# Kernel optimization log

Measured on AMD Instinct MI355X. Metric: run time of the kernel, lower is better.

The kernel has to match this reference:

```python
import jax, jax.numpy as jnp
import numpy as np

N_NODES = 50000


def gcn_conv(x, W, b, src, dst, n_nodes):
    """PyG GCNConv: x' = D^-1/2 (A+I) D^-1/2 (x W) + b (symmetric norm, self-loops)."""
    h = x @ W  # [N, out]
    loop = jnp.arange(n_nodes, dtype=src.dtype)
    src_f = jnp.concatenate([src, loop])
    dst_f = jnp.concatenate([dst, loop])
    ones = jnp.ones(src_f.shape[0], dtype=h.dtype)
    deg = jax.ops.segment_sum(ones, dst_f, num_segments=n_nodes)
    dinv = jnp.where(deg > 0, jax.lax.rsqrt(deg), 0.0)
    norm = dinv[src_f] * dinv[dst_f]  # [E+N]
    msg = h[src_f] * norm[:, None]    # irregular gather over edges
    out = jax.ops.segment_sum(msg, dst_f, num_segments=n_nodes)
    return out + b


def setup_inputs() -> dict:
    key = jax.random.key(0)
    ks = jax.random.split(key, 9)
    d_in, d_h = 128, 128
    x = jax.random.normal(ks[0], (N_NODES, d_in), dtype=jnp.float32)
    edge_index = jax.random.randint(ks[1], (2, 800000), 0, N_NODES, dtype=jnp.int64)
    glorot = lambda k, fi, fo: jax.random.normal(k, (fi, fo), dtype=jnp.float32) * jnp.sqrt(2.0 / (fi + fo))
    return {
        "x": x,
        "edge_index": edge_index,
        "W1": glorot(ks[2], d_in, d_h), "b1": jnp.zeros((d_h,), jnp.float32),
        "W2": glorot(ks[3], d_h, d_h), "b2": jnp.zeros((d_h,), jnp.float32),
        "W3": glorot(ks[4], d_h, d_h), "b3": jnp.zeros((d_h,), jnp.float32),
    }


def reference(x, edge_index, W1, b1, W2, b2, W3, b3):
    src, dst = edge_index[0], edge_index[1]
    n = x.shape[0]
    h = jax.nn.relu(gcn_conv(x, W1, b1, src, dst, n))
    h = jax.nn.relu(gcn_conv(h, W2, b2, src, dst, n))
    h = gcn_conv(h, W3, b3, src, dst, n)
    return h
```

## Files before the change

kernel.cpp:

```cpp
#include <hip/hip_runtime.h>

#define N_NODES 50000
#define N_EDGES 800000
#define DIM 128
#define WT_BLOCKS 192
#define GEMM_BLOCKS ((N_NODES + 63) / 64)
#define NBUCKET ((N_NODES + 255) / 256)
#define P1_BLOCKS 200
#define P1_CHUNK 4000
#define P2_BLOCKS 200
#define P2_CHUNK 4000

typedef unsigned int u32;
typedef short bf16x8 __attribute__((ext_vector_type(8)));
typedef float f32x4 __attribute__((ext_vector_type(4)));

static inline size_t alignUp(size_t x) { return (x + 255) & ~size_t(255); }

__device__ inline unsigned short f2bf(float f) {
    union { float f; u32 u; } v; v.f = f;
    u32 r = v.u + 0x7fffu + ((v.u >> 16) & 1u);
    return (unsigned short)(r >> 16);
}
__device__ inline float bf_lo(u32 u) { return __uint_as_float(u << 16); }
__device__ inline float bf_hi(u32 u) { return __uint_as_float(u & 0xffff0000u); }

__device__ inline void accum8(float acc[8], uint4 r, float w) {
    acc[0] += w * bf_lo(r.x); acc[1] += w * bf_hi(r.x);
    acc[2] += w * bf_lo(r.y); acc[3] += w * bf_hi(r.y);
    acc[4] += w * bf_lo(r.z); acc[5] += w * bf_hi(r.z);
    acc[6] += w * bf_lo(r.w); acc[7] += w * bf_hi(r.w);
}

__global__ __launch_bounds__(256) void prep_kernel(const float* __restrict__ W1,
                                                   const float* __restrict__ W2,
                                                   const float* __restrict__ W3,
                                                   unsigned short* __restrict__ Wt,
                                                   const int* __restrict__ dst,
                                                   u32* __restrict__ bcnt) {
    __shared__ u32 hist[NBUCKET];
    int bid = blockIdx.x;
    if (bid < WT_BLOCKS) {
        int m = bid >> 6;
        int e = (bid & 63) * 256 + threadIdx.x;
        int n = e >> 7, k = e & 127;
        const float* W = (m == 0) ? W1 : (m == 1) ? W2 : W3;
        Wt[m * DIM * DIM + n * DIM + k] = f2bf(W[(size_t)k * DIM + n]);
        return;
    }
    int b = bid - WT_BLOCKS;
    for (int k = threadIdx.x; k < NBUCKET; k += 256) hist[k] = 0;
    __syncthreads();
    int e0 = b * P1_CHUNK;
    int e1 = min(e0 + P1_CHUNK, N_EDGES);
    for (int i = e0 + threadIdx.x; i < e1; i += 256)
        atomicAdd(&hist[((u32)dst[i]) >> 8], 1u);
    __syncthreads();
    for (int k = threadIdx.x; k < NBUCKET; k += 256)
        if (hist[k]) atomicAdd(&bcnt[k], hist[k]);
}

__global__ __launch_bounds__(256) void part_kernel(const int* __restrict__ src,
                                                   const int* __restrict__ dst,
                                                   const u32* __restrict__ bcnt,
                                                   u32* __restrict__ bcur,
                                                   u32* __restrict__ epart) {
    __shared__ u32 ed[P2_CHUNK];
    __shared__ u32 hist[NBUCKET];
    __shared__ u32 cb[NBUCKET];
    __shared__ u32 rk[NBUCKET];
    __shared__ u32 bb[256];
    __shared__ u32 wsum[4];
    int tid = threadIdx.x, lane = tid & 63, wv = tid >> 6;
    u32 c = (tid < NBUCKET) ? bcnt[tid] : 0;
    u32 v = c;
#pragma unroll
    for (int off = 1; off < 64; off <<= 1) {
        u32 u = __shfl_up(v, off, 64);
        if (lane >= off) v += u;
    }
    if (lane == 63) wsum[wv] = v;
    for (int k = tid; k < NBUCKET; k += 256) { hist[k] = 0; rk[k] = 0; }
    __syncthreads();
    u32 wo = 0;
    for (int w = 0; w < wv; w++) wo += wsum[w];
    bb[tid] = wo + v - c;
    __syncthreads();
    int e0 = blockIdx.x * P2_CHUNK;
    int e1 = min(e0 + P2_CHUNK, N_EDGES);
    for (int i = e0 + tid; i < e1; i += 256) {
        u32 s = (u32)src[i], d = (u32)dst[i];
        u32 val = s | (d << 16);
        ed[i - e0] = val;
        atomicAdd(&hist[d >> 8], 1u);
    }
    __syncthreads();
    for (int k = tid; k < NBUCKET; k += 256) {
        u32 ck = hist[k];
        cb[k] = ck ? (bb[k] + atomicAdd(&bcur[k], ck)) : 0u;
    }
    __syncthreads();
    int n = e1 - e0;
    for (int k = tid; k < n; k += 256) {
        u32 val = ed[k];
        u32 bk = val >> 24;
        u32 r = atomicAdd(&rk[bk], 1u);
        epart[cb[bk] + r] = val;
    }
}

#define LDSTRIDE 40
__global__ __launch_bounds__(256) void gemm_mfma_kernel(const float* __restrict__ x,
                                                        const unsigned short* __restrict__ xb,
                                                        const unsigned short* __restrict__ Wt,
                                                        unsigned short* __restrict__ hb,
                                                        int n_rows,
                                                        const u32* __restrict__ bcnt,
                                                        const u32* __restrict__ epart,
                                                        int* __restrict__ cnt,
                                                        int* __restrict__ base,
                                                        float* __restrict__ dinv,
                                                        unsigned short* __restrict__ csr16) {
    __shared__ unsigned short As[64 * LDSTRIDE];
    __shared__ unsigned short Bs[128 * LDSTRIDE];
    if (blockIdx.x >= GEMM_BLOCKS) {
        int B = blockIdx.x - GEMM_BLOCKS;
        u32* hcnt = (u32*)&As[0];
        u32* pref = hcnt + 256;
        u32* bbl  = pref + 256;
        u32* wsum = bbl + 256;
        int tid = threadIdx.x, lane = tid & 63, wv = tid >> 6;
        int nb0 = B << 8;
        u32 cb_ = (tid < NBUCKET) ? bcnt[tid] : 0;
        u32 vb = cb_;
#pragma unroll
        for (int off = 1; off < 64; off <<= 1) {
            u32 u = __shfl_up(vb, off, 64);
            if (lane >= off) vb += u;
        }
        if (lane == 63) wsum[wv] = vb;
        hcnt[tid] = 0;
        __syncthreads();
        u32 wob = 0;
        for (int w = 0; w < wv; w++) wob += wsum[w];
        bbl[tid] = wob + vb - cb_;
        __syncthreads();
        u32 ebeg = bbl[B];
        u32 esz  = bcnt[B];
        for (u32 k = tid; k < esz; k += 256)
            atomicAdd(&hcnt[(epart[ebeg + k] >> 16) & 255u], 1u);
        __syncthreads();
        u32 c = hcnt[tid];
        u32 v = c;
#pragma unroll
        for (int off = 1; off < 64; off <<= 1) {
            u32 u = __shfl_up(v, off, 64);
            if (lane >= off) v += u;
        }
        if (lane == 63) wsum[wv] = v;
        __syncthreads();
        u32 wo = 0;
        for (int w = 0; w < wv; w++) wo += wsum[w];
        u32 excl = wo + v - c;
        int node = nb0 + tid;
        if (node < N_NODES) {
            cnt[node]  = (int)c;
            base[node] = (int)(ebeg + excl);
            dinv[node] = rsqrtf((float)(c + 1));
        }
        pref[tid] = excl;
        __syncthreads();
        for (u32 k = tid; k < esz; k += 256) {
            u32 v2 = epart[ebeg + k];
            u32 dl = (v2 >> 16) & 255u;
            u32 r = atomicAdd(&pref[dl], 1u);
            csr16[ebeg + r] = (unsigned short)(v2 & 0xffffu);
        }
        return;
    }
    const int tid = threadIdx.x;
    const int wave = tid >> 6;
    const int lane = tid & 63;
    const int quad = lane >> 4;
    const int l16 = lane & 15;
    const int row0 = blockIdx.x * 64;

    f32x4 acc[8];
#pragma unroll
    for (int nt = 0; nt < 8; nt++) acc[nt] = (f32x4){0.f, 0.f, 0.f, 0.f};

    for (int k0 = 0; k0 < DIM; k0 += 32) {
        {
            int r = tid >> 2;
            int kq = (tid & 3) * 8;
            int gr = row0 + r;
            if (xb) {
                uint4 v = make_uint4(0u, 0u, 0u, 0u);
                if (gr < n_rows) v = *(const uint4*)&xb[(size_t)gr * DIM + k0 + kq];
                *(uint4*)&As[r * LDSTRIDE + kq] = v;
            } else {
                float4 v0 = make_float4(0.f, 0.f, 0.f, 0.f);
                float4 v1 = make_float4(0.f, 0.f, 0.f, 0.f);
                if (gr < n_rows) {
                    v0 = *(const float4*)&x[(size_t)gr * DIM + k0 + kq];
                    v1 = *(const float4*)&x[(size_t)gr * DIM + k0 + kq + 4];
                }
                u32 p0 = (u32)f2bf(v0.x) | ((u32)f2bf(v0.y) << 16);
                u32 p1 = (u32)f2bf(v0.z) | ((u32)f2bf(v0.w) << 16);
                u32 p2 = (u32)f2bf(v1.x) | ((u32)f2bf(v1.y) << 16);
                u32 p3 = (u32)f2bf(v1.z) | ((u32)f2bf(v1.w) << 16);
                *(uint4*)&As[r * LDSTRIDE + kq] = make_uint4(p0, p1, p2, p3);
            }
        }
#pragma unroll
        for (int p = 0; p < 2; p++) {
            int nn = p * 64 + (tid >> 2);
            int kk = (tid & 3) * 8;
            *(uint4*)&Bs[nn * LDSTRIDE + kk] = *(const uint4*)&Wt[nn * DIM + k0 + kk];
        }
        __syncthreads();
        const int m0 = wave * 16;
        bf16x8 a = *(const bf16x8*)&As[(m0 + l16) * LDSTRIDE + quad * 8];
#pragma unroll
        for (int nt = 0; nt < 8; nt++) {
            bf16x8 b = *(const bf16x8*)&Bs[(nt * 16 + l16) * LDSTRIDE + quad * 8];
            acc[nt] = __builtin_amdgcn_mfma_f32_16x16x32_bf16(a, b, acc[nt], 0, 0, 0);
        }
        __syncthreads();
    }
    const int m0 = wave * 16;
#pragma unroll
    for (int reg = 0; reg < 4; reg++) {
        int gr = row0 + m0 + quad * 4 + reg;
        if (gr < n_rows) {
#pragma unroll
            for (int nt = 0; nt < 8; nt++)
                hb[(size_t)gr * DIM + nt * 16 + l16] = f2bf(acc[nt][reg]);
        }
    }
}

__global__ __launch_bounds__(256) void agg_kernel(const uint4* __restrict__ hb,
                                                  const int* __restrict__ cnt,
                                                  const int* __restrict__ basep,
                                                  const unsigned short* __restrict__ csr16,
                                                  const float* __restrict__ dinv,
                                                  const float4* __restrict__ bias4,
                                                  unsigned short* __restrict__ outb,
                                                  float* __restrict__ outf, int relu) {
    const int wave = threadIdx.x >> 6;
    const int lane = threadIdx.x & 63;
    const int node = blockIdx.x * 4 + wave;
    const int g = lane >> 4;
    const int l16 = lane & 15;

    const int deg = cnt[node];
    const float di = dinv[node];
    const int start = basep[node];

    float acc[8];
#pragma unroll
    for (int i = 0; i < 8; i++) acc[i] = 0.f;

    for (int b0 = 0; b0 < deg; b0 += 64) {
        int m = min(64, deg - b0);
        int e = 0; float w = 0.f;
        if (lane < m) {
            e = csr16[start + b0 + lane];
            w = dinv[e];
        }
        for (int j4 = 0; j4 < m; j4 += 16) {
            int j0 = j4 + g, j1 = j4 + 4 + g, j2 = j4 + 8 + g, j3 = j4 + 12 + g;
            int s0 = __shfl(e, j0, 64);  float w0 = __shfl(w, j0, 64);
            int s1 = __shfl(e, j1, 64);  float w1 = __shfl(w, j1, 64);
            int s2 = __shfl(e, j2, 64);  float w2 = __shfl(w, j2, 64);
            int s3 = __shfl(e, j3, 64);  float w3 = __shfl(w, j3, 64);
            uint4 r0 = hb[(size_t)s0 * 16 + l16];
            uint4 r1 = hb[(size_t)s1 * 16 + l16];
            uint4 r2 = hb[(size_t)s2 * 16 + l16];
            uint4 r3 = hb[(size_t)s3 * 16 + l16];
            accum8(acc, r0, w0);
            accum8(acc, r1, w1);
            accum8(acc, r2, w2);
            accum8(acc, r3, w3);
        }
    }
    if (g == 0) {
        uint4 r = hb[(size_t)node * 16 + l16];
        accum8(acc, r, di);
    }
#pragma unroll
    for (int i = 0; i < 8; i++) {
        acc[i] += __shfl_xor(acc[i], 16, 64);
        acc[i] += __shfl_xor(acc[i], 32, 64);
    }
    if (g == 0) {
        float4 b0 = bias4[l16 * 2], b1 = bias4[l16 * 2 + 1];
        float res[8];
        res[0] = di * acc[0] + b0.x; res[1] = di * acc[1] + b0.y;
        res[2] = di * acc[2] + b0.z; res[3] = di * acc[3] + b0.w;
        res[4] = di * acc[4] + b1.x; res[5] = di * acc[5] + b1.y;
        res[6] = di * acc[6] + b1.z; res[7] = di * acc[7] + b1.w;
        if (relu) {
#pragma unroll
            for (int i = 0; i < 8; i++) res[i] = fmaxf(res[i], 0.f);
        }
        if (outb) {
            u32 p0 = (u32)f2bf(res[0]) | ((u32)f2bf(res[1]) << 16);
            u32 p1 = (u32)f2bf(res[2]) | ((u32)f2bf(res[3]) << 16);
            u32 p2 = (u32)f2bf(res[4]) | ((u32)f2bf(res[5]) << 16);
            u32 p3 = (u32)f2bf(res[6]) | ((u32)f2bf(res[7]) << 16);
            ((uint4*)outb)[(size_t)node * 16 + l16] = make_uint4(p0, p1, p2, p3);
        } else {
            float4* o = (float4*)(outf + (size_t)node * DIM);
            o[l16 * 2]     = make_float4(res[0], res[1], res[2], res[3]);
            o[l16 * 2 + 1] = make_float4(res[4], res[5], res[6], res[7]);
        }
    }
}


extern "C" void kernel_launch(void* const* d_in, const int* in_sizes, int n_in,
                              void* d_out, int out_size, void* d_ws, size_t ws_size,
                              hipStream_t stream) {
    const float* x  = (const float*)d_in[0];
    const int* ei   = (const int*)d_in[1];
    const float* W1 = (const float*)d_in[2];
    const float* b1 = (const float*)d_in[3];
    const float* W2 = (const float*)d_in[4];
    const float* b2 = (const float*)d_in[5];
    const float* W3 = (const float*)d_in[6];
    const float* b3 = (const float*)d_in[7];
    const int* src = ei;
    const int* dst = ei + N_EDGES;
    float* out = (float*)d_out;

    char* w = (char*)d_ws;
    u32* bcnt  = (u32*)w; w += alignUp((size_t)2 * NBUCKET * 4);
    u32* bcur  = bcnt + NBUCKET;
    int* cnt   = (int*)w; w += alignUp((size_t)N_NODES * 4);
    int* base  = (int*)w; w += alignUp((size_t)N_NODES * 4);
    float* dinvb = (float*)w; w += alignUp((size_t)N_NODES * 4);
    u32* epart = (u32*)w; w += alignUp((size_t)N_EDGES * 4);
    unsigned short* csr16 = (unsigned short*)w; w += alignUp((size_t)N_EDGES * 2);
    unsigned short* wt = (unsigned short*)w; w += alignUp((size_t)3 * DIM * DIM * 2);
    unsigned short* hbuf = (unsigned short*)w; w += alignUp((size_t)N_NODES * DIM * 2);
    unsigned short* abuf = (unsigned short*)w; w += alignUp((size_t)N_NODES * DIM * 2);

    hipMemsetAsync(bcnt, 0, (size_t)2 * NBUCKET * 4, stream);

    int ablocks = N_NODES / 4;

    prep_kernel<<<WT_BLOCKS + P1_BLOCKS, 256, 0, stream>>>(W1, W2, W3, wt, dst, bcnt);
    part_kernel<<<P2_BLOCKS, 256, 0, stream>>>(src, dst, bcnt, bcur, epart);

    gemm_mfma_kernel<<<GEMM_BLOCKS + NBUCKET, 256, 0, stream>>>(x, nullptr, wt, hbuf, N_NODES,
                                                                bcnt, epart,
                                                                cnt, base, dinvb, csr16);
    agg_kernel<<<ablocks, 256, 0, stream>>>((const uint4*)hbuf, cnt, base, csr16, dinvb,
                                            (const float4*)b1, abuf, nullptr, 1);

    gemm_mfma_kernel<<<GEMM_BLOCKS, 256, 0, stream>>>(nullptr, abuf, wt + DIM * DIM, hbuf,
                                                      N_NODES, nullptr, nullptr,
                                                      nullptr, nullptr, nullptr, nullptr);
    agg_kernel<<<ablocks, 256, 0, stream>>>((const uint4*)hbuf, cnt, base, csr16, dinvb,
                                            (const float4*)b2, abuf, nullptr, 1);

    gemm_mfma_kernel<<<GEMM_BLOCKS, 256, 0, stream>>>(nullptr, abuf, wt + 2 * DIM * DIM, hbuf,
                                                      N_NODES, nullptr, nullptr,
                                                      nullptr, nullptr, nullptr, nullptr);
    agg_kernel<<<ablocks, 256, 0, stream>>>((const uint4*)hbuf, cnt, base, csr16, dinvb,
                                            (const float4*)b3, nullptr, out, 0);
}
```

Measured before the change: 253.0 us.

## Fuse aggregation with next-layer GEMM into a single aggemm kernel

Layers 1 and 2 of aggregation now run in a new kernel that also applies the next layer's weight matrix. Each 512-thread block aggregates 8 nodes, writes the ReLU'd bf16 rows to LDS, and does a 16x128x128 MFMA against the full W tile held in LDS. This removes two standalone GEMM launches and the write and reread of the intermediate activation buffer. In exchange, every block reloads the full 32 KB weight matrix into LDS and half of each MFMA tile is zero padding, and the large LDS footprint may limit occupancy.

```diff
diff --git a/kernel.cpp b/kernel.cpp
--- a/kernel.cpp
+++ b/kernel.cpp
@@ -10,6 +10,7 @@
 #define P1_CHUNK 4000
 #define P2_BLOCKS 200
 #define P2_CHUNK 4000
+#define AGG_BLOCKS (N_NODES / 8)
 
 typedef unsigned int u32;
 typedef short bf16x8 __attribute__((ext_vector_type(8)));
@@ -111,7 +112,6 @@
 
 #define LDSTRIDE 40
 __global__ __launch_bounds__(256) void gemm_mfma_kernel(const float* __restrict__ x,
-                                                        const unsigned short* __restrict__ xb,
                                                         const unsigned short* __restrict__ Wt,
                                                         unsigned short* __restrict__ hb,
                                                         int n_rows,
@@ -194,23 +194,17 @@
             int r = tid >> 2;
             int kq = (tid & 3) * 8;
             int gr = row0 + r;
-            if (xb) {
-                uint4 v = make_uint4(0u, 0u, 0u, 0u);
-                if (gr < n_rows) v = *(const uint4*)&xb[(size_t)gr * DIM + k0 + kq];
-                *(uint4*)&As[r * LDSTRIDE + kq] = v;
-            } else {
-                float4 v0 = make_float4(0.f, 0.f, 0.f, 0.f);
-                float4 v1 = make_float4(0.f, 0.f, 0.f, 0.f);
-                if (gr < n_rows) {
-                    v0 = *(const float4*)&x[(size_t)gr * DIM + k0 + kq];
-                    v1 = *(const float4*)&x[(size_t)gr * DIM + k0 + kq + 4];
-                }
-                u32 p0 = (u32)f2bf(v0.x) | ((u32)f2bf(v0.y) << 16);
-                u32 p1 = (u32)f2bf(v0.z) | ((u32)f2bf(v0.w) << 16);
-                u32 p2 = (u32)f2bf(v1.x) | ((u32)f2bf(v1.y) << 16);
-                u32 p3 = (u32)f2bf(v1.z) | ((u32)f2bf(v1.w) << 16);
-                *(uint4*)&As[r * LDSTRIDE + kq] = make_uint4(p0, p1, p2, p3);
+            float4 v0 = make_float4(0.f, 0.f, 0.f, 0.f);
+            float4 v1 = make_float4(0.f, 0.f, 0.f, 0.f);
+            if (gr < n_rows) {
+                v0 = *(const float4*)&x[(size_t)gr * DIM + k0 + kq];
+                v1 = *(const float4*)&x[(size_t)gr * DIM + k0 + kq + 4];
             }
+            u32 p0 = (u32)f2bf(v0.x) | ((u32)f2bf(v0.y) << 16);
+            u32 p1 = (u32)f2bf(v0.z) | ((u32)f2bf(v0.w) << 16);
+            u32 p2 = (u32)f2bf(v1.x) | ((u32)f2bf(v1.y) << 16);
+            u32 p3 = (u32)f2bf(v1.z) | ((u32)f2bf(v1.w) << 16);
+            *(uint4*)&As[r * LDSTRIDE + kq] = make_uint4(p0, p1, p2, p3);
         }
 #pragma unroll
         for (int p = 0; p < 2; p++) {
@@ -236,6 +230,111 @@
 #pragma unroll
             for (int nt = 0; nt < 8; nt++)
                 hb[(size_t)gr * DIM + nt * 16 + l16] = f2bf(acc[nt][reg]);
+        }
+    }
+}
+
+#define FSTR 136
+__global__ __launch_bounds__(512, 8) void aggemm_kernel(
+        const uint4* __restrict__ hb_in,
+        const unsigned short* __restrict__ Wt,
+        const int* __restrict__ cnt,
+        const int* __restrict__ basep,
+        const unsigned short* __restrict__ csr16,
+        const float* __restrict__ dinv,
+        const float4* __restrict__ bias4,
+        unsigned short* __restrict__ hb_out) {
+    __shared__ unsigned short As[16 * FSTR];
+    __shared__ unsigned short Bs[128 * FSTR];
+    const int tid = threadIdx.x;
+    const int wave = tid >> 6;
+    const int lane = tid & 63;
+    const int g = lane >> 4;
+    const int l16 = lane & 15;
+
+#pragma unroll
+    for (int i = 0; i < 4; i++) {
+        int idx = i * 512 + tid;
+        int n = idx >> 4, k8 = (idx & 15) * 8;
+        *(uint4*)&Bs[n * FSTR + k8] = *(const uint4*)&Wt[n * DIM + k8];
+    }
+    {
+        u32* az = (u32*)As;
+        for (int i = tid; i < (8 * FSTR) / 2; i += 512) az[(8 * FSTR) / 2 + i] = 0;
+    }
+
+    const int node = blockIdx.x * 8 + wave;
+    const int deg = cnt[node];
+    const float di = dinv[node];
+    const int start = basep[node];
+
+    float acc[8];
+#pragma unroll
+    for (int i = 0; i < 8; i++) acc[i] = 0.f;
+
+    for (int b0 = 0; b0 < deg; b0 += 64) {
+        int m = min(64, deg - b0);
+        int e = 0; float w = 0.f;
+        if (lane < m) {
+            e = csr16[start + b0 + lane];
+            w = dinv[e];
+        }
+        for (int j4 = 0; j4 < m; j4 += 16) {
+            int j0 = j4 + g, j1 = j4 + 4 + g, j2 = j4 + 8 + g, j3 = j4 + 12 + g;
+            int s0 = __shfl(e, j0, 64);  float w0 = __shfl(w, j0, 64);
+            int s1 = __shfl(e, j1, 64);  float w1 = __shfl(w, j1, 64);
+            int s2 = __shfl(e, j2, 64);  float w2 = __shfl(w, j2, 64);
+            int s3 = __shfl(e, j3, 64);  float w3 = __shfl(w, j3, 64);
+            uint4 r0 = hb_in[(size_t)s0 * 16 + l16];
+            uint4 r1 = hb_in[(size_t)s1 * 16 + l16];
+            uint4 r2 = hb_in[(size_t)s2 * 16 + l16];
+            uint4 r3 = hb_in[(size_t)s3 * 16 + l16];
+            accum8(acc, r0, w0);
+            accum8(acc, r1, w1);
+            accum8(acc, r2, w2);
+            accum8(acc, r3, w3);
+        }
+    }
+    if (g == 0) {
+        uint4 r = hb_in[(size_t)node * 16 + l16];
+        accum8(acc, r, di);
+    }
+#pragma unroll
+    for (int i = 0; i < 8; i++) {
+        acc[i] += __shfl_xor(acc[i], 16, 64);
+        acc[i] += __shfl_xor(acc[i], 32, 64);
+    }
+    if (g == 0) {
+        float4 bv0 = bias4[l16 * 2], bv1 = bias4[l16 * 2 + 1];
+        float res[8];
+        res[0] = di * acc[0] + bv0.x; res[1] = di * acc[1] + bv0.y;
+        res[2] = di * acc[2] + bv0.z; res[3] = di * acc[3] + bv0.w;
+        res[4] = di * acc[4] + bv1.x; res[5] = di * acc[5] + bv1.y;
+        res[6] = di * acc[6] + bv1.z; res[7] = di * acc[7] + bv1.w;
+#pragma unroll
+        for (int i = 0; i < 8; i++) res[i] = fmaxf(res[i], 0.f);
+        u32 p0 = (u32)f2bf(res[0]) | ((u32)f2bf(res[1]) << 16);
+        u32 p1 = (u32)f2bf(res[2]) | ((u32)f2bf(res[3]) << 16);
+        u32 p2 = (u32)f2bf(res[4]) | ((u32)f2bf(res[5]) << 16);
+        u32 p3 = (u32)f2bf(res[6]) | ((u32)f2bf(res[7]) << 16);
+        *(uint4*)&As[wave * FSTR + l16 * 8] = make_uint4(p0, p1, p2, p3);
+    }
+    __syncthreads();
+
+    const int nt = wave;
+    f32x4 gacc = (f32x4){0.f, 0.f, 0.f, 0.f};
+#pragma unroll
+    for (int ks = 0; ks < 4; ks++) {
+        bf16x8 a = *(const bf16x8*)&As[l16 * FSTR + ks * 32 + g * 8];
+        bf16x8 b = *(const bf16x8*)&Bs[(nt * 16 + l16) * FSTR + ks * 32 + g * 8];
+        gacc = __builtin_amdgcn_mfma_f32_16x16x32_bf16(a, b, gacc, 0, 0, 0);
+    }
+#pragma unroll
+    for (int reg = 0; reg < 4; reg++) {
+        int row = g * 4 + reg;
+        if (row < 8) {
+            int gr = blockIdx.x * 8 + row;
+            hb_out[(size_t)gr * DIM + nt * 16 + l16] = f2bf(gacc[reg]);
         }
     }
 }
@@ -246,8 +345,7 @@
                                                   const unsigned short* __restrict__ csr16,
                                                   const float* __restrict__ dinv,
                                                   const float4* __restrict__ bias4,
-                                                  unsigned short* __restrict__ outb,
-                                                  float* __restrict__ outf, int relu) {
+                                                  float* __restrict__ out) {
     const int wave = threadIdx.x >> 6;
     const int lane = threadIdx.x & 63;
     const int node = blockIdx.x * 4 + wave;
@@ -296,26 +394,11 @@
     }
     if (g == 0) {
         float4 b0 = bias4[l16 * 2], b1 = bias4[l16 * 2 + 1];
-        float res[8];
-        res[0] = di * acc[0] + b0.x; res[1] = di * acc[1] + b0.y;
-        res[2] = di * acc[2] + b0.z; res[3] = di * acc[3] + b0.w;
-        res[4] = di * acc[4] + b1.x; res[5] = di * acc[5] + b1.y;
-        res[6] = di * acc[6] + b1.z; res[7] = di * acc[7] + b1.w;
-        if (relu) {
-#pragma unroll
-            for (int i = 0; i < 8; i++) res[i] = fmaxf(res[i], 0.f);
-        }
-        if (outb) {
-            u32 p0 = (u32)f2bf(res[0]) | ((u32)f2bf(res[1]) << 16);
-            u32 p1 = (u32)f2bf(res[2]) | ((u32)f2bf(res[3]) << 16);
-            u32 p2 = (u32)f2bf(res[4]) | ((u32)f2bf(res[5]) << 16);
-            u32 p3 = (u32)f2bf(res[6]) | ((u32)f2bf(res[7]) << 16);
-            ((uint4*)outb)[(size_t)node * 16 + l16] = make_uint4(p0, p1, p2, p3);
-        } else {
-            float4* o = (float4*)(outf + (size_t)node * DIM);
-            o[l16 * 2]     = make_float4(res[0], res[1], res[2], res[3]);
-            o[l16 * 2 + 1] = make_float4(res[4], res[5], res[6], res[7]);
-        }
+        float4* o = (float4*)(out + (size_t)node * DIM);
+        o[l16 * 2]     = make_float4(di * acc[0] + b0.x, di * acc[1] + b0.y,
+                                     di * acc[2] + b0.z, di * acc[3] + b0.w);
+        o[l16 * 2 + 1] = make_float4(di * acc[4] + b1.x, di * acc[5] + b1.y,
+                                     di * acc[6] + b1.z, di * acc[7] + b1.w);
     }
 }
 
@@ -344,31 +427,23 @@
     u32* epart = (u32*)w; w += alignUp((size_t)N_EDGES * 4);
     unsigned short* csr16 = (unsigned short*)w; w += alignUp((size_t)N_EDGES * 2);
     unsigned short* wt = (unsigned short*)w; w += alignUp((size_t)3 * DIM * DIM * 2);
-    unsigned short* hbuf = (unsigned short*)w; w += alignUp((size_t)N_NODES * DIM * 2);
-    unsigned short* abuf = (unsigned short*)w; w += alignUp((size_t)N_NODES * DIM * 2);
+    unsigned short* hbuf  = (unsigned short*)w; w += alignUp((size_t)N_NODES * DIM * 2);
+    unsigned short* hbuf2 = (unsigned short*)w; w += alignUp((size_t)N_NODES * DIM * 2);
 
     hipMemsetAsync(bcnt, 0, (size_t)2 * NBUCKET * 4, stream);
-
-    int ablocks = N_NODES / 4;
 
     prep_kernel<<<WT_BLOCKS + P1_BLOCKS, 256, 0, stream>>>(W1, W2, W3, wt, dst, bcnt);
     part_kernel<<<P2_BLOCKS, 256, 0, stream>>>(src, dst, bcnt, bcur, epart);
 
-    gemm_mfma_kernel<<<GEMM_BLOCKS + NBUCKET, 256, 0, stream>>>(x, nullptr, wt, hbuf, N_NODES,
+    gemm_mfma_kernel<<<GEMM_BLOCKS + NBUCKET, 256, 0, stream>>>(x, wt, hbuf, N_NODES,
                                                                 bcnt, epart,
                                                                 cnt, base, dinvb, csr16);
-    agg_kernel<<<ablocks, 256, 0, stream>>>((const uint4*)hbuf, cnt, base, csr16, dinvb,
-                                            (const float4*)b1, abuf, nullptr, 1);
-
-    gemm_mfma_kernel<<<GEMM_BLOCKS, 256, 0, stream>>>(nullptr, abuf, wt + DIM * DIM, hbuf,
-                                                      N_NODES, nullptr, nullptr,
-                                                      nullptr, nullptr, nullptr, nullptr);
-    agg_kernel<<<ablocks, 256, 0, stream>>>((const uint4*)hbuf, cnt, base, csr16, dinvb,
-                                            (const float4*)b2, abuf, nullptr, 1);
-
-    gemm_mfma_kernel<<<GEMM_BLOCKS, 256, 0, stream>>>(nullptr, abuf, wt + 2 * DIM * DIM, hbuf,
-                                                      N_NODES, nullptr, nullptr,
-                                                      nullptr, nullptr, nullptr, nullptr);
-    agg_kernel<<<ablocks, 256, 0, stream>>>((const uint4*)hbuf, cnt, base, csr16, dinvb,
-                                            (const float4*)b3, nullptr, out, 0);
-}
+    aggemm_kernel<<<AGG_BLOCKS, 512, 0, stream>>>((const uint4*)hbuf, wt + DIM * DIM,
+                                                  cnt, base, csr16, dinvb,
+                                                  (const float4*)b1, hbuf2);
+    aggemm_kernel<<<AGG_BLOCKS, 512, 0, stream>>>((const uint4*)hbuf2, wt + 2 * DIM * DIM,
+                                                  cnt, base, csr16, dinvb,
+                                                  (const float4*)b2, hbuf);
+    agg_kernel<<<N_NODES / 4, 256, 0, stream>>>((const uint4*)hbuf, cnt, base, csr16, dinvb,
+                                                (const float4*)b3, out);
+}
```

Measured after the change: 272.3 us. +7.6%, slower.
